# Optimization experiments

Hardware: AMD Instinct MI355X
Metric: run time of the kernel (lower is better)

The kernel has to match this reference:

```python
import jax, jax.numpy as jnp
import numpy as np

NBODY = 63          # body 0 = world, body 1 = free-joint root, bodies 2..62 = hinge
NHINGE = NBODY - 2  # 61 hinge dofs -> qpos dim = 7 + 61 = 68
NSITES = 16
B = 131072


def _qmul(q1, q2):
    """Hamilton product, (w,x,y,z) convention. Broadcasts over leading dims."""
    w1, x1, y1, z1 = q1[..., 0], q1[..., 1], q1[..., 2], q1[..., 3]
    w2, x2, y2, z2 = q2[..., 0], q2[..., 1], q2[..., 2], q2[..., 3]
    return jnp.stack([
        w1 * w2 - x1 * x2 - y1 * y2 - z1 * z2,
        w1 * x2 + x1 * w2 + y1 * z2 - z1 * y2,
        w1 * y2 - x1 * z2 + y1 * w2 + z1 * x2,
        w1 * z2 + x1 * y2 - y1 * x2 + z1 * w2,
    ], axis=-1)


def _qrot(q, v):
    """Rotate v by unit quaternion q (equivalent to q*v*q^-1 sandwich)."""
    u = q[..., 1:]
    w = q[..., :1]
    t = 2.0 * jnp.cross(u, v)
    return v + w * t + jnp.cross(u, t)


def setup_inputs() -> dict:
    key = jax.random.key(0)
    ks = jax.random.split(key, 8)
    qpos = jax.random.normal(ks[0], (B, 7 + NHINGE), dtype=jnp.float32) * 0.3
    body_pos = jax.random.normal(ks[1], (NBODY, 3), dtype=jnp.float32) * 0.1
    bq = jax.random.normal(ks[2], (NBODY, 4), dtype=jnp.float32)
    body_quat = bq / jnp.linalg.norm(bq, axis=-1, keepdims=True)
    ax = jax.random.normal(ks[3], (NHINGE, 3), dtype=jnp.float32)
    hinge_axis = ax / jnp.linalg.norm(ax, axis=-1, keepdims=True)
    jnt_pos = jax.random.normal(ks[4], (NHINGE, 3), dtype=jnp.float32) * 0.05
    site_pos = jax.random.normal(ks[5], (NSITES, 3), dtype=jnp.float32) * 0.05
    body_parent = jnp.maximum(jnp.arange(NBODY, dtype=jnp.int32) - 1, 0)  # chain tree
    site_body = jax.random.randint(ks[6], (NSITES,), 1, NBODY, dtype=jnp.int32)
    return {
        'qpos': qpos, 'body_pos': body_pos, 'body_quat': body_quat,
        'hinge_axis': hinge_axis, 'jnt_pos': jnt_pos, 'site_pos': site_pos,
        'body_parent': body_parent, 'site_body': site_body,
    }


def reference(qpos, body_pos, body_quat, hinge_axis, jnt_pos, site_pos,
              body_parent, site_body):
    # Structural ints are static tree topology: pull to host for Python indexing.
    parents = np.asarray(body_parent)
    sbody = np.asarray(site_body)
    Bn = qpos.shape[0]
    nbody = body_pos.shape[0]

    wp = [None] * nbody  # per-body world position [B,3]
    wq = [None] * nbody  # per-body world quaternion [B,4]
    wp[0] = jnp.zeros((Bn, 3), dtype=qpos.dtype)
    wq[0] = jnp.broadcast_to(jnp.array([1.0, 0.0, 0.0, 0.0], dtype=qpos.dtype), (Bn, 4))

    # body 1: free joint -> root pos + normalized quat straight from qpos
    wp[1] = qpos[:, 0:3]
    q = qpos[:, 3:7]
    wq[1] = q / jnp.linalg.norm(q, axis=-1, keepdims=True)

    # hinge bodies, parents always processed before children
    for bid in range(2, nbody):
        h = bid - 2
        p = int(parents[bid])
        half = 0.5 * qpos[:, 7 + h]
        s, c = jnp.sin(half), jnp.cos(half)
        ax = hinge_axis[h]
        hq = jnp.stack([c, s * ax[0], s * ax[1], s * ax[2]], axis=-1)  # [B,4]
        local_combined = _qmul(jnp.broadcast_to(body_quat[bid], (Bn, 4)), hq)
        anchor = wp[p] + _qrot(wq[p], body_pos[bid] + jnt_pos[h])  # world joint anchor
        nq = _qmul(wq[p], local_combined)
        wq[bid] = nq
        wp[bid] = anchor - _qrot(nq, jnt_pos[h])

    WP = jnp.stack(wp, axis=1)  # [B, nbody, 3]
    WQ = jnp.stack(wq, axis=1)  # [B, nbody, 4]

    # sites: vectorized gather + rotate over all keypoint sites at once
    sq = WQ[:, sbody]                         # [B, S, 4]
    sp = WP[:, sbody]                         # [B, S, 3]
    sites = sp + _qrot(sq, site_pos[None, :, :])  # [B, S, 3]
    return sites
```

## Files before the change

kernel.cpp:

```cpp
#include <hip/hip_runtime.h>


#define NBODY  63
#define NHINGE 61
#define NSITES 16
#define QDIM   68
#define LSTRIDE 49

__global__ __launch_bounds__(256, 2)
void fk_main(const float* __restrict__ qpos,
             const float* __restrict__ body_pos,
             const float* __restrict__ body_quat,
             const float* __restrict__ hinge_axis,
             const float* __restrict__ jnt_pos,
             const float* __restrict__ site_pos,
             const int* __restrict__ site_body,
             float* __restrict__ out, int nb)
{
    __shared__ float sbuf[256 * LSTRIDE];
    __shared__ float hc[NHINGE][16];
    __shared__ float spos[NSITES][4];
    __shared__ int   smask[NBODY];

    const int tid = threadIdx.x;
    const int t = blockIdx.x * 256 + tid;
    float* my = sbuf + tid * LSTRIDE;

    float f[QDIM];
    if (t < nb) {
        const float4* q4 = reinterpret_cast<const float4*>(qpos) + (size_t)t * 17;
#pragma unroll
        for (int i = 0; i < 17; i++) {
            float4 v = q4[i];
            f[4*i+0] = v.x; f[4*i+1] = v.y; f[4*i+2] = v.z; f[4*i+3] = v.w;
        }
#pragma unroll
        for (int i = 0; i < QDIM; i++)
            asm volatile("" : "+v"(f[i]));
    }

    if (tid < NHINGE) {
        int h = tid, bid = h + 2;
        float uw = body_quat[bid*4+0], ux = body_quat[bid*4+1];
        float uy = body_quat[bid*4+2], uz = body_quat[bid*4+3];
        float ax = hinge_axis[h*3+0], ay = hinge_axis[h*3+1], az = hinge_axis[h*3+2];
        float jx = jnt_pos[h*3+0],   jy = jnt_pos[h*3+1],   jz = jnt_pos[h*3+2];
        float bx = body_pos[bid*3+0], by = body_pos[bid*3+1], bz = body_pos[bid*3+2];
        hc[h][0] = uw; hc[h][1] = ux; hc[h][2] = uy; hc[h][3] = uz;
        hc[h][4] = -(ux * ax + uy * ay + uz * az);
        hc[h][5] =  uw * ax + uy * az - uz * ay;
        hc[h][6] =  uw * ay - ux * az + uz * ax;
        hc[h][7] =  uw * az + ux * ay - uy * ax;
        hc[h][8] = bx + jx; hc[h][9] = by + jy; hc[h][10] = bz + jz; hc[h][11] = 0.f;
        hc[h][12] = jx; hc[h][13] = jy; hc[h][14] = jz; hc[h][15] = 0.f;
    }
    if (tid < NSITES) {
        spos[tid][0] = site_pos[tid*3+0];
        spos[tid][1] = site_pos[tid*3+1];
        spos[tid][2] = site_pos[tid*3+2];
        spos[tid][3] = 0.f;
    }
    if (tid < NBODY) {
        int m = 0;
#pragma unroll
        for (int s = 0; s < NSITES; s++)
            m |= (site_body[s] == tid) ? (1 << s) : 0;
        smask[tid] = m;
    }
    unsigned long long bodymask = 0ull;
#pragma unroll
    for (int s = 0; s < NSITES; s++)
        bodymask |= 1ull << site_body[s];

    __syncthreads();

    if (t < nb) {
        float wpx = f[0], wpy = f[1], wpz = f[2];
        float qw = f[3], qx = f[4], qy = f[5], qz = f[6];
        float inv = rsqrtf(qw * qw + qx * qx + qy * qy + qz * qz);
        qw *= inv; qx *= inv; qy *= inv; qz *= inv;

        auto emit = [&](int bid) {
            int m = __builtin_amdgcn_readfirstlane(smask[bid]);
            while (m) {
                int s = __ffs(m) - 1; m &= m - 1;
                float vx = spos[s][0], vy = spos[s][1], vz = spos[s][2];
                float tx = 2.f * (qy * vz - qz * vy);
                float ty = 2.f * (qz * vx - qx * vz);
                float tz = 2.f * (qx * vy - qy * vx);
                float* o = my + s * 3;
                o[0] = wpx + vx + qw * tx + (qy * tz - qz * ty);
                o[1] = wpy + vy + qw * ty + (qz * tx - qx * tz);
                o[2] = wpz + vz + qw * tz + (qx * ty - qy * tx);
            }
        };

        if (bodymask & 2ull) emit(1);

#pragma unroll
        for (int h = 0; h < NHINGE; h++) {
            const int bid = h + 2;
            const float* c = hc[h];
            float ang = 0.5f * f[7 + h];
            float sn, cs;
            __sincosf(ang, &sn, &cs);
            float lw = cs * c[0] + sn * c[4];
            float lx = cs * c[1] + sn * c[5];
            float ly = cs * c[2] + sn * c[6];
            float lz = cs * c[3] + sn * c[7];
            float ax = c[8], ay = c[9], az = c[10];
            float tx = 2.f * (qy * az - qz * ay);
            float ty = 2.f * (qz * ax - qx * az);
            float tz = 2.f * (qx * ay - qy * ax);
            float anx = wpx + ax + qw * tx + (qy * tz - qz * ty);
            float any_ = wpy + ay + qw * ty + (qz * tx - qx * tz);
            float anz = wpz + az + qw * tz + (qx * ty - qy * tx);
            float nw = qw * lw - qx * lx - qy * ly - qz * lz;
            float nx = qw * lx + qx * lw + qy * lz - qz * ly;
            float ny = qw * ly - qx * lz + qy * lw + qz * lx;
            float nz = qw * lz + qx * ly - qy * lx + qz * lw;
            float jx = c[12], jy = c[13], jz = c[14];
            float t2x = 2.f * (ny * jz - nz * jy);
            float t2y = 2.f * (nz * jx - nx * jz);
            float t2z = 2.f * (nx * jy - ny * jx);
            wpx = anx - (jx + nw * t2x + (ny * t2z - nz * t2y));
            wpy = any_ - (jy + nw * t2y + (nz * t2x - nx * t2z));
            wpz = anz - (jz + nw * t2z + (nx * t2y - ny * t2x));
            qw = nw; qx = nx; qy = ny; qz = nz;

            if (bodymask & (1ull << bid)) emit(bid);
        }
    }

    __syncthreads();

    {
        size_t blk_dw = (size_t)blockIdx.x * (256 * 48);
        if (blk_dw + 256 * 48 <= (size_t)nb * 48) {
            float4* out4 = reinterpret_cast<float4*>(out + blk_dw);
#pragma unroll
            for (int k = 0; k < 12; k++) {
                int g = k * 256 + tid;
                int q = g / 12;
                int r = (g - q * 12) * 4;
                const float* p = sbuf + q * LSTRIDE + r;
                float4 v = { p[0], p[1], p[2], p[3] };
                out4[g] = v;
            }
        } else if (t < nb) {
            for (int k = 0; k < 48; k++) out[(size_t)t * 48 + k] = my[k];
        }
    }
}

extern "C" void kernel_launch(void* const* d_in, const int* in_sizes, int n_in,
                              void* d_out, int out_size, void* d_ws, size_t ws_size,
                              hipStream_t stream)
{
    const float* qpos       = (const float*)d_in[0];
    const float* body_pos   = (const float*)d_in[1];
    const float* body_quat  = (const float*)d_in[2];
    const float* hinge_axis = (const float*)d_in[3];
    const float* jnt_pos    = (const float*)d_in[4];
    const float* site_pos   = (const float*)d_in[5];
    const int* site_body    = (const int*)d_in[7];

    int nb = in_sizes[0] / QDIM;

    fk_main<<<(nb + 255) / 256, 256, 0, stream>>>(qpos, body_pos, body_quat,
                                                  hinge_axis, jnt_pos, site_pos,
                                                  site_body, (float*)d_out, nb);
}
```

Measured before the change: 123.9 us.

## Stream qpos loads in software-pipelined chunks instead of preloading all 68 floats

After: 117.9 us. 4.8% less time.

```diff
diff --git a/kernel.cpp b/kernel.cpp
--- a/kernel.cpp
+++ b/kernel.cpp
@@ -6,6 +6,8 @@
 #define NSITES 16
 #define QDIM   68
 #define LSTRIDE 49
+
+typedef unsigned long long u64;
 
 __global__ __launch_bounds__(256, 2)
 void fk_main(const float* __restrict__ qpos,
@@ -25,19 +27,6 @@
     const int tid = threadIdx.x;
     const int t = blockIdx.x * 256 + tid;
     float* my = sbuf + tid * LSTRIDE;
-
-    float f[QDIM];
-    if (t < nb) {
-        const float4* q4 = reinterpret_cast<const float4*>(qpos) + (size_t)t * 17;
-#pragma unroll
-        for (int i = 0; i < 17; i++) {
-            float4 v = q4[i];
-            f[4*i+0] = v.x; f[4*i+1] = v.y; f[4*i+2] = v.z; f[4*i+3] = v.w;
-        }
-#pragma unroll
-        for (int i = 0; i < QDIM; i++)
-            asm volatile("" : "+v"(f[i]));
-    }
 
     if (tid < NHINGE) {
         int h = tid, bid = h + 2;
@@ -67,7 +56,7 @@
             m |= (site_body[s] == tid) ? (1 << s) : 0;
         smask[tid] = m;
     }
-    unsigned long long bodymask = 0ull;
+    u64 bodymask = 0ull;
 #pragma unroll
     for (int s = 0; s < NSITES; s++)
         bodymask |= 1ull << site_body[s];
@@ -75,8 +64,13 @@
     __syncthreads();
 
     if (t < nb) {
-        float wpx = f[0], wpy = f[1], wpz = f[2];
-        float qw = f[3], qx = f[4], qy = f[5], qz = f[6];
+        const float4* q4 = reinterpret_cast<const float4*>(qpos) + (size_t)t * 17;
+        float4 c0 = q4[0];
+        float4 c1 = q4[1];
+        float4 w0 = q4[2], w1 = q4[3], w2 = q4[4];
+
+        float wpx = c0.x, wpy = c0.y, wpz = c0.z;
+        float qw = c0.w, qx = c1.x, qy = c1.y, qz = c1.z;
         float inv = rsqrtf(qw * qw + qx * qx + qy * qy + qz * qz);
         qw *= inv; qx *= inv; qy *= inv; qz *= inv;
 
@@ -95,15 +89,10 @@
             }
         };
 
-        if (bodymask & 2ull) emit(1);
-
-#pragma unroll
-        for (int h = 0; h < NHINGE; h++) {
-            const int bid = h + 2;
+        auto hinge = [&](int h, float angle) {
             const float* c = hc[h];
-            float ang = 0.5f * f[7 + h];
             float sn, cs;
-            __sincosf(ang, &sn, &cs);
+            __sincosf(0.5f * angle, &sn, &cs);
             float lw = cs * c[0] + sn * c[4];
             float lx = cs * c[1] + sn * c[5];
             float ly = cs * c[2] + sn * c[6];
@@ -127,8 +116,31 @@
             wpy = any_ - (jy + nw * t2y + (nz * t2x - nx * t2z));
             wpz = anz - (jz + nw * t2z + (nx * t2y - ny * t2x));
             qw = nw; qx = nx; qy = ny; qz = nz;
+        };
 
-            if (bodymask & (1ull << bid)) emit(bid);
+        if (bodymask & 2ull) emit(1);
+        hinge(0, c1.w);
+        if (bodymask & 4ull) emit(2);
+
+#pragma clang loop unroll(disable)
+        for (int j = 0; j < 5; ++j) {
+            int kb = 5 + 3 * j;
+            float4 n0 = q4[kb     > 16 ? 16 : kb    ];
+            float4 n1 = q4[kb + 1 > 16 ? 16 : kb + 1];
+            float4 n2 = q4[kb + 2 > 16 ? 16 : kb + 2];
+
+            float ang[12] = { w0.x, w0.y, w0.z, w0.w,
+                              w1.x, w1.y, w1.z, w1.w,
+                              w2.x, w2.y, w2.z, w2.w };
+            int h0 = 1 + 12 * j;
+#pragma unroll
+            for (int m = 0; m < 12; ++m) {
+                int h = h0 + m;
+                hinge(h, ang[m]);
+                int bid = h + 2;
+                if ((bodymask >> bid) & 1ull) emit(bid);
+            }
+            w0 = n0; w1 = n1; w2 = n2;
         }
     }
 
```
